# Performance work log

Hardware: AMD Instinct MI355X
Metric: run time of the kernel (lower is better)

Reference implementation:

```python
import jax, jax.numpy as jnp
import numpy as np

B, T, H, I, E = 2, 2048, 1024, 2048, 8
TOP_K = 2
RMS_EPS = 1e-6
ROUTING_GAIN = 1.0
INIT_STD = 0.02


def setup_inputs() -> dict:
    key = jax.random.key(0)
    ks = jax.random.split(key, 6)
    x = jax.random.normal(ks[0], (B, T, H), dtype=jnp.float32)
    q_norm_w = jnp.ones((H,), dtype=jnp.float32)
    k_proto = jax.random.normal(ks[1], (E, H), dtype=jnp.float32) * INIT_STD
    v_proto = jnp.eye(E, dtype=jnp.float32)  # nn.init.eye_
    gate_projs = jax.random.normal(ks[2], (E, H, I), dtype=jnp.float32) * INIT_STD
    up_projs = jax.random.normal(ks[3], (E, H, I), dtype=jnp.float32) * INIT_STD
    down_projs = jax.random.normal(ks[4], (E, I, H), dtype=jnp.float32) * INIT_STD
    return {"x": x, "q_norm_w": q_norm_w, "k_proto": k_proto, "v_proto": v_proto,
            "gate_projs": gate_projs, "up_projs": up_projs, "down_projs": down_projs}


def _routing_weights(x, q_norm_w, k_proto, v_proto):
    # CAPRRouter: RMSNorm -> proto attention -> softmax -> value mix -> gain
    q = x * jax.lax.rsqrt(jnp.mean(x * x, axis=-1, keepdims=True) + RMS_EPS) * q_norm_w
    attn = jax.nn.softmax(jnp.einsum('bth,ph->btp', q, k_proto) / np.sqrt(H).astype(np.float32), axis=-1)
    logits = jnp.einsum('btp,pq->btq', attn, v_proto) * ROUTING_GAIN
    rw = jax.nn.softmax(logits, axis=-1)  # [B,T,E]
    if TOP_K < E:
        tw, ti = jax.lax.top_k(rw, TOP_K)                       # [B,T,k]
        onehot = jax.nn.one_hot(ti, E, dtype=rw.dtype)          # [B,T,k,E]
        rw = jnp.einsum('btk,btke->bte', tw, onehot)            # scatter top-k back
        rw = rw / (jnp.sum(rw, axis=-1, keepdims=True) + 1e-9)
    return rw


def reference(x, q_norm_w, k_proto, v_proto, gate_projs, up_projs, down_projs):
    rw = _routing_weights(x, q_norm_w, k_proto, v_proto)  # [B,T,E]
    # Math-equivalent reassociation of torch's ('btp,phi->bthi' then 'bth,bthi->bti'):
    # per-expert GEMM then routing-weighted reduction over experts.
    gate_out = jnp.einsum('btp,btpi->bti', rw, jnp.einsum('bth,phi->btpi', x, gate_projs))
    up_out = jnp.einsum('btp,btpi->bti', rw, jnp.einsum('bth,phi->btpi', x, up_projs))
    intermediate = jax.nn.silu(gate_out) * up_out  # [B,T,I]
    output = jnp.einsum('btp,btph->bth', rw, jnp.einsum('bti,pih->btph', intermediate, down_projs))
    return output, rw
```

## Files before the change

kernel.cpp:

```cpp
#include <hip/hip_runtime.h>
#include <hip/hip_bf16.h>

#define NTOK 4096
#define HDIM 1024
#define IDIM 2048
#define NEXP 8
#define RBLK 16

typedef __attribute__((ext_vector_type(8))) short short8;
typedef __attribute__((ext_vector_type(4))) short short4b;
typedef __attribute__((ext_vector_type(4))) float f32x4;
typedef unsigned short ushort_t;

__device__ inline ushort_t f2bf(float f) {
    union { float f; unsigned u; } v; v.f = f;
    unsigned r = v.u + 0x7FFFu + ((v.u >> 16) & 1u);
    return (ushort_t)(r >> 16);
}
__device__ inline float bf2f(ushort_t h) {
    union { unsigned u; float f; } v; v.u = ((unsigned)h) << 16;
    return v.f;
}

#define GPTR(p) ((const __attribute__((address_space(1))) void*)(p))
#define LPTR(p) ((__attribute__((address_space(3))) void*)(p))

__global__ __launch_bounds__(256) void routing_kernel(
    const float* __restrict__ x, const float* __restrict__ qw,
    const float* __restrict__ kp, const float* __restrict__ vp,
    float* __restrict__ rw_out, int* __restrict__ counts,
    int* __restrict__ list, float2* __restrict__ topw,
    ushort_t* __restrict__ xb)
{
    __shared__ float kp_s[NEXP * HDIM];
    __shared__ float vp_s[NEXP * NEXP];
    __shared__ int lcnt[NEXP];
    __shared__ int base_s[NEXP];
    __shared__ int tinfo[RBLK][4];

    int tid = threadIdx.x;
    int wid = tid >> 6, lane = tid & 63;

    if (tid < NEXP) lcnt[tid] = 0;
    if (tid < NEXP * NEXP) vp_s[tid] = vp[tid];
    #pragma unroll
    for (int i = 0; i < 8; i++)
        ((float4*)kp_s)[tid + 256 * i] = ((const float4*)kp)[tid + 256 * i];

    float4 qv[4];
    #pragma unroll
    for (int j = 0; j < 4; j++) qv[j] = ((const float4*)qw)[lane + 64 * j];
    __syncthreads();

    for (int it = 0; it < RBLK / 4; it++) {
        int tl = wid * (RBLK / 4) + it;
        int t = blockIdx.x * RBLK + tl;
        const float4* xr4 = (const float4*)(x + (size_t)t * HDIM);
        float4 xv[4];
        #pragma unroll
        for (int j = 0; j < 4; j++) xv[j] = xr4[lane + 64 * j];

        ushort_t* xrow = xb + (size_t)t * HDIM;
        #pragma unroll
        for (int j = 0; j < 4; j++) {
            short4b o;
            o[0] = f2bf(xv[j].x); o[1] = f2bf(xv[j].y);
            o[2] = f2bf(xv[j].z); o[3] = f2bf(xv[j].w);
            ((short4b*)xrow)[lane + 64 * j] = o;
        }

        float ss = 0.f;
        #pragma unroll
        for (int j = 0; j < 4; j++)
            ss += xv[j].x*xv[j].x + xv[j].y*xv[j].y + xv[j].z*xv[j].z + xv[j].w*xv[j].w;
        #pragma unroll
        for (int off = 32; off; off >>= 1) ss += __shfl_xor(ss, off);
        float rms = rsqrtf(ss * (1.0f / HDIM) + 1e-6f);

        float4 q[4];
        #pragma unroll
        for (int j = 0; j < 4; j++) {
            q[j].x = xv[j].x * rms * qv[j].x; q[j].y = xv[j].y * rms * qv[j].y;
            q[j].z = xv[j].z * rms * qv[j].z; q[j].w = xv[j].w * rms * qv[j].w;
        }

        float d[NEXP];
        #pragma unroll
        for (int p = 0; p < NEXP; p++) {
            float acc = 0.f;
            #pragma unroll
            for (int j = 0; j < 4; j++) {
                float4 kv = ((const float4*)kp_s)[p * 256 + lane + 64 * j];
                acc += q[j].x*kv.x + q[j].y*kv.y + q[j].z*kv.z + q[j].w*kv.w;
            }
            #pragma unroll
            for (int off = 32; off; off >>= 1) acc += __shfl_xor(acc, off);
            d[p] = acc * (1.0f / 32.0f);
        }

        float m = d[0];
        #pragma unroll
        for (int p = 1; p < NEXP; p++) m = fmaxf(m, d[p]);
        float a[NEXP]; float s = 0.f;
        #pragma unroll
        for (int p = 0; p < NEXP; p++) { a[p] = expf(d[p] - m); s += a[p]; }
        float inv = 1.0f / s;
        #pragma unroll
        for (int p = 0; p < NEXP; p++) a[p] *= inv;
        float lg[NEXP];
        #pragma unroll
        for (int qi = 0; qi < NEXP; qi++) {
            float acc = 0.f;
            #pragma unroll
            for (int p = 0; p < NEXP; p++) acc += a[p] * vp_s[p * NEXP + qi];
            lg[qi] = acc;
        }
        float m2 = lg[0];
        #pragma unroll
        for (int p = 1; p < NEXP; p++) m2 = fmaxf(m2, lg[p]);
        float r[NEXP]; float s2 = 0.f;
        #pragma unroll
        for (int p = 0; p < NEXP; p++) { r[p] = expf(lg[p] - m2); s2 += r[p]; }
        float inv2 = 1.0f / s2;
        #pragma unroll
        for (int p = 0; p < NEXP; p++) r[p] *= inv2;
        int e0 = -1, e1 = -1; float w0 = -1.f, w1 = -1.f;
        #pragma unroll
        for (int p = 0; p < NEXP; p++) {
            if (r[p] > w0) { w1 = w0; e1 = e0; w0 = r[p]; e0 = p; }
            else if (r[p] > w1) { w1 = r[p]; e1 = p; }
        }
        float invn = 1.0f / (w0 + w1 + 1e-9f);
        float w0n = w0 * invn, w1n = w1 * invn;

        if (lane == 0) {
            #pragma unroll
            for (int p = 0; p < NEXP; p++)
                rw_out[(size_t)t * NEXP + p] = (p == e0) ? w0n : ((p == e1) ? w1n : 0.f);
            topw[t] = make_float2(w0n, w1n);
            int p0 = atomicAdd(&lcnt[e0], 1);
            int p1 = atomicAdd(&lcnt[e1], 1);
            tinfo[tl][0] = e0; tinfo[tl][1] = p0;
            tinfo[tl][2] = e1; tinfo[tl][3] = p1;
        }
    }
    __syncthreads();
    if (tid < NEXP) base_s[tid] = atomicAdd(&counts[tid], lcnt[tid]);
    __syncthreads();
    if (tid < RBLK) {
        int t = blockIdx.x * RBLK + tid;
        int e0 = tinfo[tid][0], p0 = tinfo[tid][1];
        int e1 = tinfo[tid][2], p1 = tinfo[tid][3];
        list[e0 * NTOK + base_s[e0] + p0] = t * 2;
        list[e1 * NTOK + base_s[e1] + p1] = t * 2 + 1;
    }
}

__global__ __launch_bounds__(256) void conv_t(const float* __restrict__ in, ushort_t* __restrict__ out,
                                              int K, int N) {
    __shared__ ushort_t ts[64][72];
    int e = blockIdx.z;
    int xb = blockIdx.x, yb = blockIdx.y;
    const float* ip = in + (size_t)e * K * N + (size_t)(yb * 64) * N + xb * 64;
    int NB = N / 128, KB = K / 64;
    int nb = xb >> 1, rhalf = (xb & 1) * 64;
    ushort_t* op = out + ((size_t)((size_t)e * NB + nb) * KB + yb) * (128 * 64);

    int tid = threadIdx.x;
    int r0 = tid >> 4;
    int c4 = (tid & 15) * 4;
    #pragma unroll
    for (int i = 0; i < 4; i++) {
        int r = r0 + i * 16;
        float4 v = *(const float4*)(ip + (size_t)r * N + c4);
        ts[c4+0][r] = f2bf(v.x); ts[c4+1][r] = f2bf(v.y);
        ts[c4+2][r] = f2bf(v.z); ts[c4+3][r] = f2bf(v.w);
    }
    __syncthreads();
    int n = tid >> 2;
    int kq = (tid & 3) * 16;
    int sw = (n & 7) << 3;
    short8 w0 = *(const short8*)&ts[n][kq];
    short8 w1 = *(const short8*)&ts[n][kq + 8];
    ushort_t* dst = op + (size_t)(rhalf + n) * 64;
    *(short8*)(dst + (kq ^ sw))       = w0;
    *(short8*)(dst + ((kq + 8) ^ sw)) = w1;
}

template<int KLEN, int KTOT, int FUSED, int OUTBF, int SPLITK>
__global__ __launch_bounds__(256) void gemm_bf16(
    const ushort_t* __restrict__ A,
    const ushort_t* __restrict__ W0, const ushort_t* __restrict__ W1,
    const int* __restrict__ counts, const int* __restrict__ list,
    void* __restrict__ out0, void* __restrict__ out1, int odim)
{
    constexpr int KB = KLEN / 64;
    constexpr int KBTOT = KTOT / 64;
    int zz = blockIdx.z;
    int e      = SPLITK ? (zz & (NEXP - 1)) : zz;
    int ksplit = SPLITK ? (zz >> 3) : 0;
    int koff   = ksplit * KLEN;

    int M = counts[e];
    int row0 = blockIdx.y * 128;
    if (row0 >= M) return;
    int nbTiles = odim / 128;
    int colb = blockIdx.x;
    const ushort_t* W = (FUSED && colb >= nbTiles) ? W1 : W0;
    void* outp        = (FUSED && colb >= nbTiles) ? out1 : out0;
    int nb = (FUSED && colb >= nbTiles) ? colb - nbTiles : colb;
    int col0 = nb * 128;

    __shared__ ushort_t Abuf[128 * 64];
    __shared__ ushort_t Bbuf[128 * 64];
    __shared__ int rowsS[128];

    int tid = threadIdx.x;
    if (tid < 128) {
        int r = row0 + tid;
        rowsS[tid] = (r < M) ? list[e * NTOK + r] : -1;
    }
    __syncthreads();

    int wid = tid >> 6, lane = tid & 63;
    int wr = wid >> 1, wc = wid & 1;
    int la = lane & 15, lb = lane >> 4;

    int swu = ((((lane & 7) * 16) ^ ((lane >> 3) << 4)) >> 1);
    const ushort_t* aP[4];
    #pragma unroll
    for (int i = 0; i < 4; i++) {
        int r = (wid * 4 + i) * 8 + (lane >> 3);
        int ent = rowsS[r];
        int tok = (ent >= 0) ? (ent >> 1) : 0;
        aP[i] = A + (size_t)tok * KTOT + koff + swu;
    }
    const ushort_t* Wt = W + (size_t)((size_t)e * nbTiles + nb) * ((size_t)KBTOT * 8192)
                           + (size_t)(koff / 64) * 8192;

    int swr = (la & 7) << 3;
    int aoff[4][2], boff[4][2];
    #pragma unroll
    for (int m = 0; m < 4; m++)
        #pragma unroll
        for (int ks = 0; ks < 2; ks++)
            aoff[m][ks] = (wr * 64 + m * 16 + la) * 64 + ((ks * 32 + lb * 8) ^ swr);
    #pragma unroll
    for (int n = 0; n < 4; n++)
        #pragma unroll
        for (int ks = 0; ks < 2; ks++)
            boff[n][ks] = (wc * 64 + n * 16 + la) * 64 + ((ks * 32 + lb * 8) ^ swr);

    f32x4 acc[4][4];
    #pragma unroll
    for (int m = 0; m < 4; m++)
        #pragma unroll
        for (int n = 0; n < 4; n++) acc[m][n] = (f32x4){0.f, 0.f, 0.f, 0.f};

    for (int kt = 0; kt < KB; kt++) {
        #pragma unroll
        for (int i = 0; i < 4; i++) {
            int seg = wid * 4 + i;
            __builtin_amdgcn_global_load_lds(GPTR(aP[i] + kt * 64),
                                             LPTR(Abuf + seg * 512), 16, 0, 0);
            __builtin_amdgcn_global_load_lds(GPTR(Wt + (size_t)kt * 8192 + seg * 512 + lane * 8),
                                             LPTR(Bbuf + seg * 512), 16, 0, 0);
        }
        __syncthreads();
        #pragma unroll
        for (int ks = 0; ks < 2; ks++) {
            short8 af[4], bf[4];
            #pragma unroll
            for (int m = 0; m < 4; m++) af[m] = *(const short8*)&Abuf[aoff[m][ks]];
            #pragma unroll
            for (int n = 0; n < 4; n++) bf[n] = *(const short8*)&Bbuf[boff[n][ks]];
            #pragma unroll
            for (int m = 0; m < 4; m++)
                #pragma unroll
                for (int n = 0; n < 4; n++)
                    acc[m][n] = __builtin_amdgcn_mfma_f32_16x16x32_bf16(af[m], bf[n], acc[m][n], 0, 0, 0);
        }
        __syncthreads();
    }

    #pragma unroll
    for (int m = 0; m < 4; m++) {
        #pragma unroll
        for (int j = 0; j < 4; j++) {
            int rl = wr * 64 + m * 16 + lb * 4 + j;
            int ent = rowsS[rl];
            if (ent >= 0) {
                size_t base = (size_t)ent * odim + col0 + wc * 64 + la;
                #pragma unroll
                for (int n = 0; n < 4; n++) {
                    if (OUTBF) {
                        ((ushort_t*)outp)[base + n * 16] = f2bf(acc[m][n][j]);
                    } else {
                        float* oF = (float*)outp + (size_t)ksplit * 2 * NTOK * odim;
                        oF[base + n * 16] = acc[m][n][j];
                    }
                }
            }
        }
    }
}

__global__ __launch_bounds__(256) void silu_mix(
    const ushort_t* __restrict__ bg, const ushort_t* __restrict__ bu,
    const float2* __restrict__ topw, ushort_t* __restrict__ inter)
{
    int idx = blockIdx.x * 256 + threadIdx.x;
    int t = idx >> 8;
    int i8 = (idx & 255) * 8;
    float2 w = topw[t];
    short8 g0 = *(const short8*)(bg + (size_t)(2*t)   * IDIM + i8);
    short8 g1 = *(const short8*)(bg + (size_t)(2*t+1) * IDIM + i8);
    short8 u0 = *(const short8*)(bu + (size_t)(2*t)   * IDIM + i8);
    short8 u1 = *(const short8*)(bu + (size_t)(2*t+1) * IDIM + i8);
    short8 r;
    #pragma unroll
    for (int j = 0; j < 8; j++) {
        float g = w.x * bf2f((ushort_t)g0[j]) + w.y * bf2f((ushort_t)g1[j]);
        float u = w.x * bf2f((ushort_t)u0[j]) + w.y * bf2f((ushort_t)u1[j]);
        float s = g / (1.f + expf(-g)) * u;
        r[j] = f2bf(s);
    }
    *(short8*)(inter + (size_t)t * IDIM + i8) = r;
}

__global__ __launch_bounds__(256) void out_mix(
    const float* __restrict__ pout, const float2* __restrict__ topw,
    float* __restrict__ out)
{
    const size_t SPLITSZ = (size_t)2 * NTOK * HDIM;
    int idx = blockIdx.x * 256 + threadIdx.x;
    int t = idx >> 8;
    int h4 = (idx & 255) * 4;
    float2 w = topw[t];
    float4 a0 = *(const float4*)(pout + (size_t)(2*t)   * HDIM + h4);
    float4 b0 = *(const float4*)(pout + (size_t)(2*t+1) * HDIM + h4);
    float4 a1 = *(const float4*)(pout + SPLITSZ + (size_t)(2*t)   * HDIM + h4);
    float4 b1 = *(const float4*)(pout + SPLITSZ + (size_t)(2*t+1) * HDIM + h4);
    float4 r;
    r.x = w.x*(a0.x + a1.x) + w.y*(b0.x + b1.x);
    r.y = w.x*(a0.y + a1.y) + w.y*(b0.y + b1.y);
    r.z = w.x*(a0.z + a1.z) + w.y*(b0.z + b1.z);
    r.w = w.x*(a0.w + a1.w) + w.y*(b0.w + b1.w);
    *(float4*)(out + (size_t)t * HDIM + h4) = r;
}

extern "C" void kernel_launch(void* const* d_in, const int* in_sizes, int n_in,
                              void* d_out, int out_size, void* d_ws, size_t ws_size,
                              hipStream_t stream) {
    const float* x    = (const float*)d_in[0];
    const float* qw   = (const float*)d_in[1];
    const float* kp   = (const float*)d_in[2];
    const float* vp   = (const float*)d_in[3];
    const float* gate = (const float*)d_in[4];
    const float* up   = (const float*)d_in[5];
    const float* down = (const float*)d_in[6];
    float* out = (float*)d_out;
    float* rw_out = out + (size_t)NTOK * HDIM;

    char* ws = (char*)d_ws;
    int*      counts = (int*)ws;
    float2*   topw   = (float2*)(ws + 1024);
    int*      list   = (int*)(ws + 64 * 1024);
    ushort_t* xb     = (ushort_t*)(ws + 256 * 1024);
    ushort_t* wtg    = xb + (size_t)NTOK * HDIM;
    ushort_t* wtu    = wtg + (size_t)NEXP * HDIM * IDIM;
    ushort_t* wtd    = wtu + (size_t)NEXP * HDIM * IDIM;
    ushort_t* bg     = wtd + (size_t)NEXP * HDIM * IDIM;
    ushort_t* bu     = bg  + (size_t)2 * NTOK * IDIM;
    ushort_t* interb = bu  + (size_t)2 * NTOK * IDIM;
    float*    pout   = (float*)bg;

    hipMemsetAsync(counts, 0, NEXP * sizeof(int), stream);

    routing_kernel<<<NTOK / RBLK, 256, 0, stream>>>(x, qw, kp, vp, rw_out, counts, list, topw, xb);

    conv_t<<<dim3(IDIM / 64, HDIM / 64, NEXP), 256, 0, stream>>>(gate, wtg, HDIM, IDIM);
    conv_t<<<dim3(IDIM / 64, HDIM / 64, NEXP), 256, 0, stream>>>(up,   wtu, HDIM, IDIM);
    conv_t<<<dim3(HDIM / 64, IDIM / 64, NEXP), 256, 0, stream>>>(down, wtd, IDIM, HDIM);

    dim3 ggu(2 * IDIM / 128, NTOK / 128, NEXP);
    gemm_bf16<HDIM, HDIM, 1, 1, 0><<<ggu, 256, 0, stream>>>(xb, wtg, wtu, counts, list, bg, bu, IDIM);

    silu_mix<<<NTOK * IDIM / 8 / 256, 256, 0, stream>>>(bg, bu, topw, interb);

    dim3 gd(HDIM / 128, NTOK / 128, 2 * NEXP);
    gemm_bf16<IDIM / 2, IDIM, 0, 0, 1><<<gd, 256, 0, stream>>>(interb, wtd, (const ushort_t*)nullptr,
                                                               counts, list, pout, nullptr, HDIM);

    out_mix<<<NTOK * HDIM / 4 / 256, 256, 0, stream>>>(pout, topw, out);
}
```

Before: 267.1 us.

## Use 3-stage LDS pipeline with 128x256 tiles and 8 waves in expert GEMMs

Replaces the single-buffered grouped GEMM with a triple-buffered version. Global-to-LDS loads are issued two k-steps ahead, and only a partial vmcnt wait plus a barrier runs per step. The N tile widens to 256 with 512 threads, and the weight conversion layout is changed to match. s_setprio is raised around the MFMA block. The aim is to hide global load latency and improve weight reuse, at the cost of much more LDS (about 144KB), one block per CU, and fewer blocks for the down GEMM.

```diff
diff --git a/kernel.cpp b/kernel.cpp
--- a/kernel.cpp
+++ b/kernel.cpp
@@ -162,9 +162,9 @@
     int e = blockIdx.z;
     int xb = blockIdx.x, yb = blockIdx.y;
     const float* ip = in + (size_t)e * K * N + (size_t)(yb * 64) * N + xb * 64;
-    int NB = N / 128, KB = K / 64;
-    int nb = xb >> 1, rhalf = (xb & 1) * 64;
-    ushort_t* op = out + ((size_t)((size_t)e * NB + nb) * KB + yb) * (128 * 64);
+    int NB = N / 256, KB = K / 64;
+    int nb = xb >> 2, rq = (xb & 3) * 64;
+    ushort_t* op = out + ((size_t)((size_t)e * NB + nb) * KB + yb) * 16384;
 
     int tid = threadIdx.x;
     int r0 = tid >> 4;
@@ -182,13 +182,13 @@
     int sw = (n & 7) << 3;
     short8 w0 = *(const short8*)&ts[n][kq];
     short8 w1 = *(const short8*)&ts[n][kq + 8];
-    ushort_t* dst = op + (size_t)(rhalf + n) * 64;
+    ushort_t* dst = op + (size_t)(rq + n) * 64;
     *(short8*)(dst + (kq ^ sw))       = w0;
     *(short8*)(dst + ((kq + 8) ^ sw)) = w1;
 }
 
 template<int KLEN, int KTOT, int FUSED, int OUTBF, int SPLITK>
-__global__ __launch_bounds__(256) void gemm_bf16(
+__global__ __launch_bounds__(512, 1) void gemm3s(
     const ushort_t* __restrict__ A,
     const ushort_t* __restrict__ W0, const ushort_t* __restrict__ W1,
     const int* __restrict__ counts, const int* __restrict__ list,
@@ -204,15 +204,15 @@
     int M = counts[e];
     int row0 = blockIdx.y * 128;
     if (row0 >= M) return;
-    int nbTiles = odim / 128;
+    int nbTiles = odim / 256;
     int colb = blockIdx.x;
     const ushort_t* W = (FUSED && colb >= nbTiles) ? W1 : W0;
     void* outp        = (FUSED && colb >= nbTiles) ? out1 : out0;
     int nb = (FUSED && colb >= nbTiles) ? colb - nbTiles : colb;
-    int col0 = nb * 128;
-
-    __shared__ ushort_t Abuf[128 * 64];
-    __shared__ ushort_t Bbuf[128 * 64];
+    int col0 = nb * 256;
+
+    __shared__ ushort_t LdsA[3][128 * 64];
+    __shared__ ushort_t LdsB[3][256 * 64];
     __shared__ int rowsS[128];
 
     int tid = threadIdx.x;
@@ -223,76 +223,95 @@
     __syncthreads();
 
     int wid = tid >> 6, lane = tid & 63;
-    int wr = wid >> 1, wc = wid & 1;
+    int wr = wid >> 2, wc = wid & 3;
     int la = lane & 15, lb = lane >> 4;
 
-    int swu = ((((lane & 7) * 16) ^ ((lane >> 3) << 4)) >> 1);
-    const ushort_t* aP[4];
-    #pragma unroll
-    for (int i = 0; i < 4; i++) {
-        int r = (wid * 4 + i) * 8 + (lane >> 3);
-        int ent = rowsS[r];
+    int sw8 = ((lane & 7) ^ ((lane >> 3) & 7)) * 8;
+    const ushort_t* aP[2];
+    #pragma unroll
+    for (int i = 0; i < 2; ++i) {
+        int row = i * 64 + wid * 8 + (lane >> 3);
+        int ent = rowsS[row];
         int tok = (ent >= 0) ? (ent >> 1) : 0;
-        aP[i] = A + (size_t)tok * KTOT + koff + swu;
-    }
-    const ushort_t* Wt = W + (size_t)((size_t)e * nbTiles + nb) * ((size_t)KBTOT * 8192)
-                           + (size_t)(koff / 64) * 8192;
-
-    int swr = (la & 7) << 3;
+        aP[i] = A + (size_t)tok * KTOT + koff + sw8;
+    }
+    const ushort_t* Wt = W + ((size_t)e * nbTiles + nb) * ((size_t)KBTOT * 16384)
+                           + (size_t)(koff / 64) * 16384;
+
     int aoff[4][2], boff[4][2];
     #pragma unroll
-    for (int m = 0; m < 4; m++)
-        #pragma unroll
-        for (int ks = 0; ks < 2; ks++)
-            aoff[m][ks] = (wr * 64 + m * 16 + la) * 64 + ((ks * 32 + lb * 8) ^ swr);
-    #pragma unroll
-    for (int n = 0; n < 4; n++)
-        #pragma unroll
-        for (int ks = 0; ks < 2; ks++)
-            boff[n][ks] = (wc * 64 + n * 16 + la) * 64 + ((ks * 32 + lb * 8) ^ swr);
+    for (int m = 0; m < 4; ++m)
+        #pragma unroll
+        for (int ks = 0; ks < 2; ++ks)
+            aoff[m][ks] = (wr * 64 + m * 16 + la) * 64 + ((ks * 32 + lb * 8) ^ ((la & 7) << 3));
+    #pragma unroll
+    for (int n = 0; n < 4; ++n)
+        #pragma unroll
+        for (int ks = 0; ks < 2; ++ks)
+            boff[n][ks] = (wc * 64 + n * 16 + la) * 64 + ((ks * 32 + lb * 8) ^ ((la & 7) << 3));
 
     f32x4 acc[4][4];
     #pragma unroll
-    for (int m = 0; m < 4; m++)
-        #pragma unroll
-        for (int n = 0; n < 4; n++) acc[m][n] = (f32x4){0.f, 0.f, 0.f, 0.f};
-
-    for (int kt = 0; kt < KB; kt++) {
-        #pragma unroll
-        for (int i = 0; i < 4; i++) {
-            int seg = wid * 4 + i;
-            __builtin_amdgcn_global_load_lds(GPTR(aP[i] + kt * 64),
-                                             LPTR(Abuf + seg * 512), 16, 0, 0);
-            __builtin_amdgcn_global_load_lds(GPTR(Wt + (size_t)kt * 8192 + seg * 512 + lane * 8),
-                                             LPTR(Bbuf + seg * 512), 16, 0, 0);
-        }
-        __syncthreads();
-        #pragma unroll
-        for (int ks = 0; ks < 2; ks++) {
-            short8 af[4], bf[4];
-            #pragma unroll
-            for (int m = 0; m < 4; m++) af[m] = *(const short8*)&Abuf[aoff[m][ks]];
-            #pragma unroll
-            for (int n = 0; n < 4; n++) bf[n] = *(const short8*)&Bbuf[boff[n][ks]];
-            #pragma unroll
-            for (int m = 0; m < 4; m++)
+    for (int m = 0; m < 4; ++m)
+        #pragma unroll
+        for (int n = 0; n < 4; ++n) acc[m][n] = (f32x4){0.f, 0.f, 0.f, 0.f};
+
+    auto STAGE = [&](int kt, int d) {
+        #pragma unroll
+        for (int i = 0; i < 2; ++i)
+            __builtin_amdgcn_global_load_lds(GPTR(aP[i] + (size_t)kt * 64),
+                LPTR(&LdsA[d][(i * 512 + wid * 64) * 8]), 16, 0, 0);
+        #pragma unroll
+        for (int i = 0; i < 4; ++i)
+            __builtin_amdgcn_global_load_lds(GPTR(Wt + (size_t)kt * 16384 + (i * 512 + tid) * 8),
+                LPTR(&LdsB[d][(i * 512 + wid * 64) * 8]), 16, 0, 0);
+    };
+
+    STAGE(0, 0);
+    STAGE(1, 1);
+    asm volatile("s_waitcnt vmcnt(6)" ::: "memory");
+    __builtin_amdgcn_s_barrier();
+
+    for (int t = 0; t < KB; ++t) {
+        int src = (t + 2 < KB) ? t + 2 : t;
+        STAGE(src, (t + 2) % 3);
+        const ushort_t* Ab = LdsA[t % 3];
+        const ushort_t* Bb = LdsB[t % 3];
+        short8 af[4][2], bfg[4][2];
+        #pragma unroll
+        for (int m = 0; m < 4; ++m)
+            #pragma unroll
+            for (int ks = 0; ks < 2; ++ks)
+                af[m][ks] = *(const short8*)&Ab[aoff[m][ks]];
+        #pragma unroll
+        for (int n = 0; n < 4; ++n)
+            #pragma unroll
+            for (int ks = 0; ks < 2; ++ks)
+                bfg[n][ks] = *(const short8*)&Bb[boff[n][ks]];
+        __builtin_amdgcn_s_setprio(1);
+        #pragma unroll
+        for (int m = 0; m < 4; ++m)
+            #pragma unroll
+            for (int n = 0; n < 4; ++n)
                 #pragma unroll
-                for (int n = 0; n < 4; n++)
-                    acc[m][n] = __builtin_amdgcn_mfma_f32_16x16x32_bf16(af[m], bf[n], acc[m][n], 0, 0, 0);
-        }
-        __syncthreads();
-    }
-
-    #pragma unroll
-    for (int m = 0; m < 4; m++) {
-        #pragma unroll
-        for (int j = 0; j < 4; j++) {
+                for (int ks = 0; ks < 2; ++ks)
+                    acc[m][n] = __builtin_amdgcn_mfma_f32_16x16x32_bf16(
+                        af[m][ks], bfg[n][ks], acc[m][n], 0, 0, 0);
+        __builtin_amdgcn_s_setprio(0);
+        asm volatile("s_waitcnt vmcnt(6)" ::: "memory");
+        __builtin_amdgcn_s_barrier();
+    }
+
+    #pragma unroll
+    for (int m = 0; m < 4; ++m) {
+        #pragma unroll
+        for (int j = 0; j < 4; ++j) {
             int rl = wr * 64 + m * 16 + lb * 4 + j;
             int ent = rowsS[rl];
             if (ent >= 0) {
                 size_t base = (size_t)ent * odim + col0 + wc * 64 + la;
                 #pragma unroll
-                for (int n = 0; n < 4; n++) {
+                for (int n = 0; n < 4; ++n) {
                     if (OUTBF) {
                         ((ushort_t*)outp)[base + n * 16] = f2bf(acc[m][n][j]);
                     } else {
@@ -383,14 +402,14 @@
     conv_t<<<dim3(IDIM / 64, HDIM / 64, NEXP), 256, 0, stream>>>(up,   wtu, HDIM, IDIM);
     conv_t<<<dim3(HDIM / 64, IDIM / 64, NEXP), 256, 0, stream>>>(down, wtd, IDIM, HDIM);
 
-    dim3 ggu(2 * IDIM / 128, NTOK / 128, NEXP);
-    gemm_bf16<HDIM, HDIM, 1, 1, 0><<<ggu, 256, 0, stream>>>(xb, wtg, wtu, counts, list, bg, bu, IDIM);
+    dim3 ggu(2 * IDIM / 256, NTOK / 128, NEXP);
+    gemm3s<HDIM, HDIM, 1, 1, 0><<<ggu, 512, 0, stream>>>(xb, wtg, wtu, counts, list, bg, bu, IDIM);
 
     silu_mix<<<NTOK * IDIM / 8 / 256, 256, 0, stream>>>(bg, bu, topw, interb);
 
-    dim3 gd(HDIM / 128, NTOK / 128, 2 * NEXP);
-    gemm_bf16<IDIM / 2, IDIM, 0, 0, 1><<<gd, 256, 0, stream>>>(interb, wtd, (const ushort_t*)nullptr,
-                                                               counts, list, pout, nullptr, HDIM);
+    dim3 gd(HDIM / 256, NTOK / 128, 2 * NEXP);
+    gemm3s<IDIM / 2, IDIM, 0, 0, 1><<<gd, 512, 0, stream>>>(interb, wtd, (const ushort_t*)nullptr,
+                                                            counts, list, pout, nullptr, HDIM);
 
     out_mix<<<NTOK * HDIM / 4 / 256, 256, 0, stream>>>(pout, topw, out);
 }
```

After: 311.5 us. 1.17x slower.
